# Kernel tuning notes

Hardware: AMD Instinct MI355X
Metric: run time of the kernel (lower is better)

The kernel has to match this reference:

```python
import jax, jax.numpy as jnp
import numpy as np

C = 64
CQ = C // 8
B, D, H, W = 4, 16, 16, 16


def setup_inputs() -> dict:
    key = jax.random.key(0)
    ks = jax.random.split(key, 8)
    s = 1.0 / np.sqrt(C)
    return {
        "x": jax.random.normal(ks[0], (B, C, D, H, W), jnp.float32),
        "Wq": jax.random.normal(ks[1], (CQ, C), jnp.float32) * s,
        "bq": jax.random.normal(ks[2], (CQ,), jnp.float32) * 0.01,
        "Wk": jax.random.normal(ks[3], (CQ, C), jnp.float32) * s,
        "bk": jax.random.normal(ks[4], (CQ,), jnp.float32) * 0.01,
        "Wv": jax.random.normal(ks[5], (C, C), jnp.float32) * s,
        "bv": jax.random.normal(ks[6], (C,), jnp.float32) * 0.01,
        "gamma": jnp.zeros((1,), jnp.float32) + 0.5,
    }


def reference(x, Wq, bq, Wk, bk, Wv, bv, gamma):
    b, c, d, h, w = x.shape
    n = d * h * w
    xf = x.reshape(b, c, n)  # [b, c, n]
    # 1x1x1 Conv3d == pointwise linear over channel dim
    q = jnp.einsum('oc,bcn->bon', Wq, xf) + bq[None, :, None]  # [b, cq, n]
    k = jnp.einsum('oc,bcn->bon', Wk, xf) + bk[None, :, None]  # [b, cq, n]
    v = jnp.einsum('oc,bcn->bon', Wv, xf) + bv[None, :, None]  # [b, c, n]
    # attn[b, i, j] = softmax_j(q[:, :, i] . k[:, :, j])
    scores = jnp.einsum('bci,bcj->bij', q, k)  # [b, n, n]
    attn = jax.nn.softmax(scores, axis=-1)
    # out = v @ attn^T : out[b, c, i] = sum_j v[b, c, j] * attn[b, i, j]
    out = jnp.einsum('bcj,bij->bci', v, attn).reshape(b, c, d, h, w)
    return gamma * out + x
```

## Files before the change

kernel.cpp:

```cpp
#include <hip/hip_runtime.h>
#include <hip/hip_bf16.h>
#include <cmath>

#define NTOK 4096

typedef float        f32x16 __attribute__((ext_vector_type(16)));
typedef short        s16x8  __attribute__((ext_vector_type(8)));
typedef unsigned int u32x4  __attribute__((ext_vector_type(4)));

__device__ __forceinline__ unsigned short f2bf(float f) {
    __hip_bfloat16 h = __float2bfloat16(f);
    return *reinterpret_cast<unsigned short*>(&h);
}
__device__ __forceinline__ float bf2f(unsigned short u) {
    __hip_bfloat16 h = *reinterpret_cast<__hip_bfloat16*>(&u);
    return __bfloat162float(h);
}
__device__ __forceinline__ unsigned pk2(float a, float b) {
    __hip_bfloat162 h = __float22bfloat162_rn(make_float2(a, b));
    return *reinterpret_cast<unsigned*>(&h);
}

__global__ __launch_bounds__(256)
void qkv_kernel(const float* __restrict__ x,
                const float* __restrict__ Wq, const float* __restrict__ bq,
                const float* __restrict__ Wk, const float* __restrict__ bk,
                const float* __restrict__ Wv, const float* __restrict__ bv,
                unsigned short* __restrict__ qt2, unsigned short* __restrict__ kt2,
                unsigned short* __restrict__ vt)
{
    __shared__ float wlds[8 * 64];
    __shared__ float blds[8];
    __shared__ float pacc[4][64][9];

    const int t    = threadIdx.x;
    const int lane = t & 63;
    const int wv   = t >> 6;
    const int part = blockIdx.x >> 8;
    const int vg   = blockIdx.x & 255;

    if (t < 128) {
        const int row  = t >> 4;
        const int col4 = t & 15;
        const int g    = part * 8 + row;
        const float* src = (g < 8)  ? (Wq + g * 64)
                         : (g < 16) ? (Wk + (g - 8) * 64)
                                    : (Wv + (g - 16) * 64);
        ((float4*)wlds)[t] = ((const float4*)src)[col4];
        if (t < 8) {
            const int gg = part * 8 + t;
            blds[t] = (gg < 8) ? bq[gg] : (gg < 16) ? bk[gg - 8] : bv[gg - 16];
        }
    }
    __syncthreads();

    const int gid = vg * 64 + lane;
    const int b = gid >> 12;
    const int i = gid & (NTOK - 1);

    const float* xb = x + ((size_t)b * 64 + 16 * wv) * NTOK + i;
    float xv[16];
    #pragma unroll
    for (int c = 0; c < 16; c++) xv[c] = xb[(size_t)c * NTOK];

    float a[8];
    #pragma unroll
    for (int o = 0; o < 8; o++) a[o] = 0.f;
    #pragma unroll
    for (int c4 = 0; c4 < 4; c4++) {
        #pragma unroll
        for (int o = 0; o < 8; o++) {
            const float4 wv4 = ((const float4*)wlds)[o * 16 + wv * 4 + c4];
            a[o] += wv4.x * xv[c4*4+0] + wv4.y * xv[c4*4+1]
                  + wv4.z * xv[c4*4+2] + wv4.w * xv[c4*4+3];
        }
    }
    #pragma unroll
    for (int o = 0; o < 8; o++) pacc[wv][lane][o] = a[o];
    __syncthreads();

    const int ob = 2 * wv;
    float fin[2];
    #pragma unroll
    for (int oo = 0; oo < 2; oo++)
        fin[oo] = ((pacc[0][lane][ob + oo] + pacc[1][lane][ob + oo])
                +  (pacc[2][lane][ob + oo] + pacc[3][lane][ob + oo]))
                + blds[ob + oo];

    const size_t row = (size_t)b * NTOK + i;
    if (part < 2) {
        if (part == 0) {
            const float LOG2E = 1.4426950408889634f;
            fin[0] *= LOG2E; fin[1] *= LOG2E;
        }
        unsigned short hu[2], lu[2];
        #pragma unroll
        for (int oo = 0; oo < 2; oo++) {
            hu[oo] = f2bf(fin[oo]);
            lu[oo] = f2bf(fin[oo] - bf2f(hu[oo]));
        }
        unsigned short* dst = (part == 0 ? qt2 : kt2) + row * 16 + ob;
        *(unsigned*)dst       = *(const unsigned*)hu;
        *(unsigned*)(dst + 8) = *(const unsigned*)lu;
    } else {
        const int jl   = i & 15;
        const int slot = (jl & 3) | ((jl & 4) << 1) | ((jl & 8) >> 1);
        const int cbase = (part - 2) * 8 + ob;
        unsigned short* vdst =
            vt + ((size_t)b * 256 + (i >> 4)) * 1024 + (size_t)cbase * 16 + slot;
        vdst[0]  = f2bf(fin[0]);
        vdst[16] = f2bf(fin[1]);
    }
}

__global__ __launch_bounds__(1024)
void attn_kernel(const unsigned short* __restrict__ qt2,
                 const unsigned short* __restrict__ kt2,
                 const unsigned short* __restrict__ vt,
                 const float* __restrict__ x,
                 const float* __restrict__ gamma,
                 float* __restrict__ out)
{
    __shared__ float slds[4][64][64];
    __shared__ float sldl[4][64];

    const int t    = threadIdx.x;
    const int l    = t & 63;
    const int wv   = t >> 6;
    const int qt   = wv & 1;
    const int u    = wv >> 1;
    const int lo31 = l & 31;
    const int h    = l >> 5;
    const int w     = blockIdx.x;
    const int b     = w >> 6;
    const int qbase = (w & 63) << 6;
    const int j0    = u << 9;

    const unsigned short* qrow =
        qt2 + ((size_t)b * NTOK + qbase + qt * 32 + lo31) * 16;
    s16x8 qB1 = *(const s16x8*)qrow;
    s16x8 qB2;
    if (h == 0) qB2 = *(const s16x8*)(qrow + 8);
    else        { u32x4 z = {0,0,0,0}; qB2 = __builtin_bit_cast(s16x8, z); }

    const unsigned short* kb  = kt2 + (size_t)b * NTOK * 16 + (size_t)h * 8;
    const unsigned short* vbA = vt + (size_t)b * NTOK * 64 + (size_t)lo31 * 16 + 8 * h;
    const unsigned short* vbB = vbA + 512;

    f32x16 accA, accB;
    #pragma unroll
    for (int r = 0; r < 16; r++) { accA[r] = 0.f; accB[r] = 0.f; }
    float lsum = 0.f;

    s16x8 K[2], V00[2], V01[2], V10[2], V11[2];

    #define LOADSET(s_, a_) do {                                              \
        K[s_]   = *(const s16x8*)(kb + (size_t)(j0 + ((a_) << 5) + lo31) * 16);  \
        V00[s_] = *(const s16x8*)(vbA + (size_t)((j0 >> 4) + ((a_) << 1)) * 1024);     \
        V01[s_] = *(const s16x8*)(vbA + (size_t)((j0 >> 4) + ((a_) << 1) + 1) * 1024); \
        V10[s_] = *(const s16x8*)(vbB + (size_t)((j0 >> 4) + ((a_) << 1)) * 1024);     \
        V11[s_] = *(const s16x8*)(vbB + (size_t)((j0 >> 4) + ((a_) << 1) + 1) * 1024); \
    } while (0)

    LOADSET(0, 0);

    #pragma unroll
    for (int it = 0; it < 16; ++it) {
        const int cu = it & 1;
        const int nx = it + 1;
        LOADSET(cu ^ 1, (nx < 16) ? nx : 0);

        f32x16 s;
        #pragma unroll
        for (int r = 0; r < 16; r++) s[r] = 0.f;
        s = __builtin_amdgcn_mfma_f32_32x32x16_bf16(K[cu], qB1, s, 0, 0, 0);
        s = __builtin_amdgcn_mfma_f32_32x32x16_bf16(K[cu], qB2, s, 0, 0, 0);

        #pragma unroll
        for (int r = 0; r < 16; r++) s[r] = __builtin_amdgcn_exp2f(s[r]);

        lsum += ((s[0]+s[1])+(s[2]+s[3])) + ((s[4]+s[5])+(s[6]+s[7]))
              + ((s[8]+s[9])+(s[10]+s[11])) + ((s[12]+s[13])+(s[14]+s[15]));

        u32x4 wa, wc;
        wa.x = pk2(s[0], s[1]);   wa.y = pk2(s[2], s[3]);
        wa.z = pk2(s[4], s[5]);   wa.w = pk2(s[6], s[7]);
        wc.x = pk2(s[8], s[9]);   wc.y = pk2(s[10], s[11]);
        wc.z = pk2(s[12], s[13]); wc.w = pk2(s[14], s[15]);
        s16x8 pf0 = __builtin_bit_cast(s16x8, wa);
        s16x8 pf1 = __builtin_bit_cast(s16x8, wc);

        __builtin_amdgcn_s_setprio(1);
        accA = __builtin_amdgcn_mfma_f32_32x32x16_bf16(V00[cu], pf0, accA, 0, 0, 0);
        accA = __builtin_amdgcn_mfma_f32_32x32x16_bf16(V01[cu], pf1, accA, 0, 0, 0);
        accB = __builtin_amdgcn_mfma_f32_32x32x16_bf16(V10[cu], pf0, accB, 0, 0, 0);
        accB = __builtin_amdgcn_mfma_f32_32x32x16_bf16(V11[cu], pf1, accB, 0, 0, 0);
        __builtin_amdgcn_s_setprio(0);
    }

    lsum += __shfl_xor(lsum, 32);

    #define WR_SLOT(sidx) do {                                                \
        const int s_ = (sidx);                                                \
        _Pragma("unroll")                                                     \
        for (int r = 0; r < 16; r++) {                                        \
            const int c_ = (r & 3) + 8 * (r >> 2) + 4 * h;                    \
            slds[s_][c_][qt * 32 + lo31]      = accA[r];                      \
            slds[s_][c_ + 32][qt * 32 + lo31] = accB[r];                      \
        }                                                                     \
        if (h == 0) sldl[s_][qt * 32 + lo31] = lsum;                          \
    } while (0)

    #define MRG_SLOT(sidx) do {                                               \
        const int s_ = (sidx);                                                \
        _Pragma("unroll")                                                     \
        for (int r = 0; r < 16; r++) {                                        \
            const int c_ = (r & 3) + 8 * (r >> 2) + 4 * h;                    \
            accA[r] += slds[s_][c_][qt * 32 + lo31];                          \
            accB[r] += slds[s_][c_ + 32][qt * 32 + lo31];                     \
        }                                                                     \
        lsum += sldl[s_][qt * 32 + lo31];                                     \
    } while (0)

    if (u >= 4) WR_SLOT(u - 4);
    __syncthreads();
    if (u < 4) MRG_SLOT(u);
    __syncthreads();
    if (u == 2 || u == 3) WR_SLOT(u - 2);
    __syncthreads();
    if (u < 2) MRG_SLOT(u);
    __syncthreads();
    if (u == 1) WR_SLOT(0);
    __syncthreads();
    if (u == 0) { MRG_SLOT(0); WR_SLOT(0); }
    __syncthreads();

    const int c  = t >> 4;
    const int q4 = (t & 15) << 2;
    const float g = gamma[0];
    const float4 a4 = *(const float4*)&slds[0][c][q4];
    const float g0 = g / sldl[0][q4 + 0];
    const float g1 = g / sldl[0][q4 + 1];
    const float g2 = g / sldl[0][q4 + 2];
    const float g3 = g / sldl[0][q4 + 3];
    const size_t off = (((size_t)b * 64 + c) << 12) + qbase + q4;
    const float4 xv4 = *(const float4*)(x + off);
    float4 o;
    o.x = a4.x * g0 + xv4.x;
    o.y = a4.y * g1 + xv4.y;
    o.z = a4.z * g2 + xv4.z;
    o.w = a4.w * g3 + xv4.w;
    *(float4*)(out + off) = o;
}

extern "C" void kernel_launch(void* const* d_in, const int* in_sizes, int n_in,
                              void* d_out, int out_size, void* d_ws, size_t ws_size,
                              hipStream_t stream) {
    const float* x     = (const float*)d_in[0];
    const float* Wq    = (const float*)d_in[1];
    const float* bq    = (const float*)d_in[2];
    const float* Wk    = (const float*)d_in[3];
    const float* bk    = (const float*)d_in[4];
    const float* Wv    = (const float*)d_in[5];
    const float* bv    = (const float*)d_in[6];
    const float* gamma = (const float*)d_in[7];
    float* out = (float*)d_out;

    unsigned short* qt2 = (unsigned short*)d_ws;
    unsigned short* kt2 = qt2 + (size_t)4 * NTOK * 16;
    unsigned short* vt  = kt2 + (size_t)4 * NTOK * 16;

    qkv_kernel<<<2560, 256, 0, stream>>>(x, Wq, bq, Wk, bk, Wv, bv, qt2, kt2, vt);
    attn_kernel<<<256, 1024, 0, stream>>>(qt2, kt2, vt, x, gamma, out);
}
```

Before: 31.92 us.

## Restructure QKV projection so each block computes all output channels for 32 tokens

The QKV projection kernel previously launched 2560 blocks, each computing 8 output channels for 64 tokens, so every x column was reloaded ten times. Now 512 blocks of 512 threads each load all 80 weight rows into LDS, read x once per token, and loop over five chunks of output channels with two chunk-pairs in flight. This removes the redundant global reads of x but adds more LDS reduction barriers per block, and the stores become scalar 16-bit writes instead of packed 32-bit writes.

```diff
diff --git a/kernel.cpp b/kernel.cpp
--- a/kernel.cpp
+++ b/kernel.cpp
@@ -21,7 +21,7 @@
     return *reinterpret_cast<unsigned*>(&h);
 }
 
-__global__ __launch_bounds__(256)
+__global__ __launch_bounds__(512)
 void qkv_kernel(const float* __restrict__ x,
                 const float* __restrict__ Wq, const float* __restrict__ bq,
                 const float* __restrict__ Wk, const float* __restrict__ bk,
@@ -29,87 +29,81 @@
                 unsigned short* __restrict__ qt2, unsigned short* __restrict__ kt2,
                 unsigned short* __restrict__ vt)
 {
-    __shared__ float wlds[8 * 64];
-    __shared__ float blds[8];
-    __shared__ float pacc[4][64][9];
-
-    const int t    = threadIdx.x;
-    const int lane = t & 63;
-    const int wv   = t >> 6;
-    const int part = blockIdx.x >> 8;
-    const int vg   = blockIdx.x & 255;
-
-    if (t < 128) {
-        const int row  = t >> 4;
-        const int col4 = t & 15;
-        const int g    = part * 8 + row;
-        const float* src = (g < 8)  ? (Wq + g * 64)
-                         : (g < 16) ? (Wk + (g - 8) * 64)
-                                    : (Wv + (g - 16) * 64);
-        ((float4*)wlds)[t] = ((const float4*)src)[col4];
-        if (t < 8) {
-            const int gg = part * 8 + t;
-            blds[t] = (gg < 8) ? bq[gg] : (gg < 16) ? bk[gg - 8] : bv[gg - 16];
+    __shared__ float wlds[80 * 64];
+    __shared__ float blds[80];
+    __shared__ float pacc[2][4][32][9];
+
+    const int t  = threadIdx.x;
+    const int l  = t & 63;
+    const int wv = t >> 6;
+    const int cq = wv & 3;
+    const int cp = wv >> 2;
+    const int v  = l & 31;
+    const int hh = l >> 5;
+
+    for (int idx = t; idx < 1280; idx += 512) {
+        const int row  = idx >> 4;
+        const int col4 = idx & 15;
+        const float* src = (row < 8)  ? (Wq + row * 64)
+                         : (row < 16) ? (Wk + (row - 8) * 64)
+                                      : (Wv + (row - 16) * 64);
+        ((float4*)wlds)[idx] = ((const float4*)src)[col4];
+    }
+    if (t < 80)
+        blds[t] = (t < 8) ? bq[t] : (t < 16) ? bk[t - 8] : bv[t - 16];
+    __syncthreads();
+
+    const int vg = blockIdx.x;
+    const int b  = vg >> 7;
+    const int i  = ((vg & 127) << 5) + v;
+
+    const float* xb = x + ((size_t)b * 64 + 16 * cq) * NTOK + i;
+    float xv[16];
+    #pragma unroll
+    for (int c = 0; c < 16; c++) xv[c] = xb[(size_t)c * NTOK];
+
+    const size_t row = (size_t)b * NTOK + i;
+    const int jl   = i & 15;
+    const int slot = (jl & 3) | ((jl & 4) << 1) | ((jl & 8) >> 1);
+
+    #pragma unroll
+    for (int s = 0; s < 5; ++s) {
+        const int chunk = cp + 2 * s;
+
+        float a[4];
+        #pragma unroll
+        for (int k = 0; k < 4; k++) a[k] = 0.f;
+        #pragma unroll
+        for (int c4 = 0; c4 < 4; c4++) {
+            #pragma unroll
+            for (int k = 0; k < 4; k++) {
+                const float4 w4v =
+                    ((const float4*)wlds)[(chunk * 8 + 4 * hh + k) * 16 + cq * 4 + c4];
+                a[k] += w4v.x * xv[c4*4+0] + w4v.y * xv[c4*4+1]
+                      + w4v.z * xv[c4*4+2] + w4v.w * xv[c4*4+3];
+            }
         }
-    }
-    __syncthreads();
-
-    const int gid = vg * 64 + lane;
-    const int b = gid >> 12;
-    const int i = gid & (NTOK - 1);
-
-    const float* xb = x + ((size_t)b * 64 + 16 * wv) * NTOK + i;
-    float xv[16];
-    #pragma unroll
-    for (int c = 0; c < 16; c++) xv[c] = xb[(size_t)c * NTOK];
-
-    float a[8];
-    #pragma unroll
-    for (int o = 0; o < 8; o++) a[o] = 0.f;
-    #pragma unroll
-    for (int c4 = 0; c4 < 4; c4++) {
-        #pragma unroll
-        for (int o = 0; o < 8; o++) {
-            const float4 wv4 = ((const float4*)wlds)[o * 16 + wv * 4 + c4];
-            a[o] += wv4.x * xv[c4*4+0] + wv4.y * xv[c4*4+1]
-                  + wv4.z * xv[c4*4+2] + wv4.w * xv[c4*4+3];
+        if (s) __syncthreads();
+        #pragma unroll
+        for (int k = 0; k < 4; k++) pacc[cp][cq][v][4 * hh + k] = a[k];
+        __syncthreads();
+
+        const int o = 2 * cq + hh;
+        float fin = ((pacc[cp][0][v][o] + pacc[cp][1][v][o])
+                  +  (pacc[cp][2][v][o] + pacc[cp][3][v][o]))
+                  + blds[chunk * 8 + o];
+
+        if (chunk < 2) {
+            if (chunk == 0) fin *= 1.4426950408889634f;
+            const unsigned short hu = f2bf(fin);
+            const unsigned short lu = f2bf(fin - bf2f(hu));
+            unsigned short* dst = (chunk == 0 ? qt2 : kt2) + row * 16;
+            dst[o]     = hu;
+            dst[8 + o] = lu;
+        } else {
+            const int c = (chunk - 2) * 8 + o;
+            vt[((size_t)b * 256 + (i >> 4)) * 1024 + (size_t)c * 16 + slot] = f2bf(fin);
         }
-    }
-    #pragma unroll
-    for (int o = 0; o < 8; o++) pacc[wv][lane][o] = a[o];
-    __syncthreads();
-
-    const int ob = 2 * wv;
-    float fin[2];
-    #pragma unroll
-    for (int oo = 0; oo < 2; oo++)
-        fin[oo] = ((pacc[0][lane][ob + oo] + pacc[1][lane][ob + oo])
-                +  (pacc[2][lane][ob + oo] + pacc[3][lane][ob + oo]))
-                + blds[ob + oo];
-
-    const size_t row = (size_t)b * NTOK + i;
-    if (part < 2) {
-        if (part == 0) {
-            const float LOG2E = 1.4426950408889634f;
-            fin[0] *= LOG2E; fin[1] *= LOG2E;
-        }
-        unsigned short hu[2], lu[2];
-        #pragma unroll
-        for (int oo = 0; oo < 2; oo++) {
-            hu[oo] = f2bf(fin[oo]);
-            lu[oo] = f2bf(fin[oo] - bf2f(hu[oo]));
-        }
-        unsigned short* dst = (part == 0 ? qt2 : kt2) + row * 16 + ob;
-        *(unsigned*)dst       = *(const unsigned*)hu;
-        *(unsigned*)(dst + 8) = *(const unsigned*)lu;
-    } else {
-        const int jl   = i & 15;
-        const int slot = (jl & 3) | ((jl & 4) << 1) | ((jl & 8) >> 1);
-        const int cbase = (part - 2) * 8 + ob;
-        unsigned short* vdst =
-            vt + ((size_t)b * 256 + (i >> 4)) * 1024 + (size_t)cbase * 16 + slot;
-        vdst[0]  = f2bf(fin[0]);
-        vdst[16] = f2bf(fin[1]);
     }
 }
 
@@ -270,6 +264,6 @@
     unsigned short* kt2 = qt2 + (size_t)4 * NTOK * 16;
     unsigned short* vt  = kt2 + (size_t)4 * NTOK * 16;
 
-    qkv_kernel<<<2560, 256, 0, stream>>>(x, Wq, bq, Wk, bk, Wv, bv, qt2, kt2, vt);
+    qkv_kernel<<<512, 512, 0, stream>>>(x, Wq, bq, Wk, bk, Wv, bv, qt2, kt2, vt);
     attn_kernel<<<256, 1024, 0, stream>>>(qt2, kt2, vt, x, gamma, out);
 }
```

After: 33.82 us. 1.06x slower.
